# Optimization experiments

Measured on AMD Instinct MI355X. Metric: run time of the kernel, lower is better.

The kernel has to match this reference:

```python
import jax, jax.numpy as jnp
import numpy as np

MOMENTUM = 0.9
BN_EPS = 1e-5
NORM_EPS = 1e-12
NUM_CLASSES = 10000
DIM_MLP = 512
NUM_EXPERTS = 3
FEAT_DIM = 256
N = 4096


def _l2norm(x, axis=-1):
    # F.normalize: x / max(||x||, eps)
    n = jnp.sqrt(jnp.sum(x * x, axis=axis, keepdims=True))
    return x / jnp.maximum(n, NORM_EPS)


def setup_inputs() -> dict:
    key = jax.random.key(0)
    ks = jax.random.split(key, 8)
    feat_in = jax.random.normal(ks[0], (N, DIM_MLP * NUM_EXPERTS), dtype=jnp.float32)
    label = jax.random.randint(ks[1], (N,), 0, NUM_CLASSES, dtype=jnp.int32)
    # encoder params
    W1 = jax.random.normal(ks[2], (DIM_MLP * NUM_EXPERTS, DIM_MLP), dtype=jnp.float32) / np.sqrt(DIM_MLP * NUM_EXPERTS)
    b1 = jnp.zeros((DIM_MLP,), dtype=jnp.float32)
    gamma = jnp.ones((DIM_MLP,), dtype=jnp.float32)
    beta = jnp.zeros((DIM_MLP,), dtype=jnp.float32)
    W2 = jax.random.normal(ks[3], (DIM_MLP, FEAT_DIM), dtype=jnp.float32) / np.sqrt(DIM_MLP)
    b2 = jnp.zeros((FEAT_DIM,), dtype=jnp.float32)
    # memory bank buffer: randn then row-normalized (as in __init__)
    memory_pt = _l2norm(jax.random.normal(ks[4], (NUM_CLASSES, FEAT_DIM), dtype=jnp.float32))
    return {"feat_in": feat_in, "label": label, "W1": W1, "b1": b1,
            "gamma": gamma, "beta": beta, "W2": W2, "b2": b2,
            "memory_pt": memory_pt}


def _encoder(feat_in, W1, b1, gamma, beta, W2, b2):
    h = feat_in @ W1 + b1                       # [N, dim_mlp]
    # BatchNorm1d in training mode: batch statistics (biased variance)
    mu = jnp.mean(h, axis=0)
    var = jnp.mean((h - mu) ** 2, axis=0)
    h = (h - mu) * jax.lax.rsqrt(var + BN_EPS) * gamma + beta
    h = jax.nn.relu(h)
    out = h @ W2 + b2                           # [N, 256]
    return _l2norm(out, axis=1)


def _update_memory(memory_pt, feat, label):
    # Strictly sequential per-sample momentum update (order matters for
    # duplicate labels), each touched row renormalized — lax.scan recurrence.
    def step(mem, xy):
        x, y = xy
        pt = MOMENTUM * mem[y] + (1.0 - MOMENTUM) * x
        pt = _l2norm(pt, axis=0)
        return mem.at[y].set(pt), None
    mem, _ = jax.lax.scan(step, memory_pt, (feat, label))
    return mem


def reference(feat_in, label, W1, b1, gamma, beta, W2, b2, memory_pt):
    feat = _encoder(feat_in, W1, b1, gamma, beta, W2, b2)   # [N, 256], unit rows
    # memory_pt.detach(): no grad flows through the memory bank
    mem = _update_memory(jax.lax.stop_gradient(memory_pt),
                         jax.lax.stop_gradient(feat), label)
    mem = jax.lax.stop_gradient(mem)
    sim_logit = jnp.einsum('nc,kc->nk', feat, mem)          # [N, K]
    return sim_logit
```

## Files before the change

### kernel.cpp

```cpp
#include <hip/hip_runtime.h>
#include <stdint.h>

typedef _Float16 f16;
typedef _Float16 f16x2 __attribute__((ext_vector_type(2)));
typedef _Float16 f16x4 __attribute__((ext_vector_type(4)));
typedef _Float16 f16x8 __attribute__((ext_vector_type(8)));
typedef float f32x4 __attribute__((ext_vector_type(4)));

typedef __attribute__((address_space(1))) void gvoid;
typedef __attribute__((address_space(3))) void lvoid;

#define NROWS 4096
#define DIMIN 1536
#define DMLP 512
#define FDIM 256
#define NCLS 10000
#define NPAD 10112

__device__ __forceinline__ void load_lds16(const void* g, void* l) {
    __builtin_amdgcn_global_load_lds((gvoid*)g, (lvoid*)l, 16, 0, 0);
}

template<int TM, int TN>
__global__ __launch_bounds__(256) void gemm_t(
    const f16* __restrict__ A, const f16* __restrict__ Bt,
    float* __restrict__ C, const float* __restrict__ bias,
    int K, int ldc, int Nstore)
{
    constexpr int BK = 64;
    constexpr int AM = TM / 32;
    constexpr int AN = TN / 32;
    constexpr int CA = TM * 8;
    constexpr int CB = TN * 8;
    constexpr int RTOT = (CA + CB) / 256;

    __shared__ f16 As[TM * BK];
    __shared__ f16 Bs[TN * BK];

    const int tid  = threadIdx.x;
    const int lane = tid & 63;
    const int w    = tid >> 6;
    const int wm   = (w >> 1) * (TM / 2);
    const int wn   = (w & 1) * (TN / 2);
    const int row0 = blockIdx.x * TM;
    const int col0 = blockIdx.y * TN;
    const int quad = lane >> 4;
    const int r16  = lane & 15;

    f32x4 acc[AM][AN] = {};

    const f16* gsrc[RTOT];
    f16* ldst[RTOT];
#pragma unroll
    for (int r = 0; r < RTOT; ++r) {
        int c = tid + r * 256;
        bool isA = (c < CA);
        int cc = isA ? c : c - CA;
        int row = cc >> 3;
        int gs = (cc & 7) ^ (row & 7);
        gsrc[r] = (isA ? A + (size_t)(row0 + row) * K
                       : Bt + (size_t)(col0 + row) * K) + gs * 8;
        ldst[r] = (isA ? As : Bs) + cc * 8;
    }

    for (int k0 = 0; k0 < K; k0 += BK) {
#pragma unroll
        for (int r = 0; r < RTOT; ++r)
            load_lds16(gsrc[r] + k0, ldst[r]);
        __syncthreads();

#pragma unroll
        for (int ks = 0; ks < 2; ++ks) {
            f16x8 af[AM], bq[AN];
#pragma unroll
            for (int mi = 0; mi < AM; ++mi) {
                int row = wm + mi * 16 + r16;
                int slot = (ks * 4 + quad) ^ (r16 & 7);
                af[mi] = *(const f16x8*)&As[row * BK + slot * 8];
            }
#pragma unroll
            for (int ni = 0; ni < AN; ++ni) {
                int row = wn + ni * 16 + r16;
                int slot = (ks * 4 + quad) ^ (r16 & 7);
                bq[ni] = *(const f16x8*)&Bs[row * BK + slot * 8];
            }
#pragma unroll
            for (int mi = 0; mi < AM; ++mi)
#pragma unroll
                for (int ni = 0; ni < AN; ++ni)
                    acc[mi][ni] = __builtin_amdgcn_mfma_f32_16x16x32_f16(
                        af[mi], bq[ni], acc[mi][ni], 0, 0, 0);
        }
        __syncthreads();
    }

#pragma unroll
    for (int mi = 0; mi < AM; ++mi) {
#pragma unroll
        for (int ni = 0; ni < AN; ++ni) {
            int col = col0 + wn + ni * 16 + r16;
            if (col < Nstore) {
                float bv = bias ? bias[col] : 0.0f;
                int rowb = row0 + wm + mi * 16 + quad * 4;
#pragma unroll
                for (int r = 0; r < 4; ++r)
                    C[(size_t)(rowb + r) * ldc + col] = acc[mi][ni][r] + bv;
            }
        }
    }
}

__global__ void zero_k(float* __restrict__ p, int n) {
    int i = blockIdx.x * 256 + threadIdx.x;
    if (i < n) p[i] = 0.0f;
}

__global__ void f32_to_f16_k(const float* __restrict__ in, f16* __restrict__ out, int n4) {
    int i = blockIdx.x * 256 + threadIdx.x;
    if (i >= n4) return;
    float4 v = *(const float4*)&in[(size_t)i * 4];
    f16x4 o = {(f16)v.x, (f16)v.y, (f16)v.z, (f16)v.w};
    *(f16x4*)&out[(size_t)i * 4] = o;
}

__global__ void transpose_to_f16_k(const float* __restrict__ in, f16* __restrict__ out, int R, int C) {
    int idx = blockIdx.x * 256 + threadIdx.x;
    if (idx >= R * C) return;
    int n = idx / R, k = idx - n * R;
    out[idx] = (f16)in[(size_t)k * C + n];
}

__global__ void bn_stats_k(const float* __restrict__ h, float* __restrict__ sums, float* __restrict__ sqs) {
    int t = threadIdx.x, b = blockIdx.x;
    int c = t * 2;
    float s0 = 0.f, s1 = 0.f, q0 = 0.f, q1 = 0.f;
    for (int r = b; r < NROWS; r += 128) {
        float2 v = *(const float2*)&h[(size_t)r * DMLP + c];
        s0 += v.x; s1 += v.y; q0 += v.x * v.x; q1 += v.y * v.y;
    }
    atomicAdd(&sums[c], s0);
    atomicAdd(&sums[c + 1], s1);
    atomicAdd(&sqs[c], q0);
    atomicAdd(&sqs[c + 1], q1);
}

__global__ void bn_finish_k(const float* __restrict__ sums, const float* __restrict__ sqs,
                            const float* __restrict__ gamma, const float* __restrict__ beta,
                            float* __restrict__ scale, float* __restrict__ shift) {
    int c = blockIdx.x * 256 + threadIdx.x;
    if (c >= DMLP) return;
    const float inv_n = 1.0f / 4096.0f;
    float mu = sums[c] * inv_n;
    float var = fmaxf(sqs[c] * inv_n - mu * mu, 0.0f);
    float a = rsqrtf(var + 1e-5f) * gamma[c];
    scale[c] = a;
    shift[c] = beta[c] - mu * a;
}

__global__ void bn_apply_k(const float* __restrict__ h, const float* __restrict__ scale,
                           const float* __restrict__ shift, f16* __restrict__ out) {
    int i = blockIdx.x * 256 + threadIdx.x;
    int c = (i & 127) * 4;
    float4 v = *(const float4*)&h[(size_t)i * 4];
    float4 sc = *(const float4*)&scale[c];
    float4 sh = *(const float4*)&shift[c];
    f16x4 o = {(f16)fmaxf(v.x * sc.x + sh.x, 0.0f),
               (f16)fmaxf(v.y * sc.y + sh.y, 0.0f),
               (f16)fmaxf(v.z * sc.z + sh.z, 0.0f),
               (f16)fmaxf(v.w * sc.w + sh.w, 0.0f)};
    *(f16x4*)&out[(size_t)i * 4] = o;
}

__global__ void l2norm_k(const float* __restrict__ X, float* __restrict__ Y, f16* __restrict__ Yh) {
    int wv = (blockIdx.x * 256 + threadIdx.x) >> 6;
    int lane = threadIdx.x & 63;
    float4 v = *(const float4*)&X[(size_t)wv * FDIM + lane * 4];
    float s = v.x * v.x + v.y * v.y + v.z * v.z + v.w * v.w;
#pragma unroll
    for (int off = 32; off > 0; off >>= 1) s += __shfl_xor(s, off);
    float inv = 1.0f / fmaxf(sqrtf(s), 1e-12f);
    float4 o = {v.x * inv, v.y * inv, v.z * inv, v.w * inv};
    *(float4*)&Y[(size_t)wv * FDIM + lane * 4] = o;
    f16x4 oh = {(f16)o.x, (f16)o.y, (f16)o.z, (f16)o.w};
    *(f16x4*)&Yh[(size_t)wv * FDIM + lane * 4] = oh;
}

__global__ void chain_k(const int* __restrict__ label, const float* __restrict__ feat,
                        const float* __restrict__ mp, f16* __restrict__ memh) {
    int y = (blockIdx.x * 256 + threadIdx.x) >> 6;
    int lane = threadIdx.x & 63;
    float4 m = {0.f, 0.f, 0.f, 0.f};
    if (y < NCLS) {
        m = *(const float4*)&mp[(size_t)y * FDIM + lane * 4];
        for (int g = 0; g < 64; ++g) {
            int lab = label[g * 64 + lane];
            unsigned long long mask = __ballot(lab == y);
            while (mask) {
                int b = __builtin_ctzll(mask);
                mask &= mask - 1;
                int i = g * 64 + b;
                float4 x = *(const float4*)&feat[(size_t)i * FDIM + lane * 4];
                m.x = 0.9f * m.x + 0.1f * x.x;
                m.y = 0.9f * m.y + 0.1f * x.y;
                m.z = 0.9f * m.z + 0.1f * x.z;
                m.w = 0.9f * m.w + 0.1f * x.w;
                float s = m.x * m.x + m.y * m.y + m.z * m.z + m.w * m.w;
#pragma unroll
                for (int off = 32; off > 0; off >>= 1) s += __shfl_xor(s, off);
                float inv = 1.0f / fmaxf(sqrtf(s), 1e-12f);
                m.x *= inv; m.y *= inv; m.z *= inv; m.w *= inv;
            }
        }
    }
    f16x4 o = {(f16)m.x, (f16)m.y, (f16)m.z, (f16)m.w};
    *(f16x4*)&memh[(size_t)y * FDIM + lane * 4] = o;
}

extern "C" void kernel_launch(void* const* d_in, const int* in_sizes, int n_in,
                              void* d_out, int out_size, void* d_ws, size_t ws_size,
                              hipStream_t stream) {
    const float* feat_in = (const float*)d_in[0];
    const int*   label   = (const int*)d_in[1];
    const float* W1      = (const float*)d_in[2];
    const float* b1      = (const float*)d_in[3];
    const float* gamma   = (const float*)d_in[4];
    const float* beta    = (const float*)d_in[5];
    const float* W2      = (const float*)d_in[6];
    const float* b2      = (const float*)d_in[7];
    const float* mp      = (const float*)d_in[8];
    float* out = (float*)d_out;

    char* w = (char*)d_ws;
    f16* A1h   = (f16*)w;   w += (size_t)NROWS * DIMIN * 2;
    f16* W1t   = (f16*)w;   w += (size_t)DMLP * DIMIN * 2;
    f16* W2t   = (f16*)w;   w += (size_t)FDIM * DMLP * 2;
    float* h   = (float*)w; w += (size_t)NROWS * DMLP * 4;
    f16* h2    = (f16*)w;   w += (size_t)NROWS * DMLP * 2;
    float* out2= (float*)w; w += (size_t)NROWS * FDIM * 4;
    float* feat= (float*)w; w += (size_t)NROWS * FDIM * 4;
    f16* feath = (f16*)w;   w += (size_t)NROWS * FDIM * 2;
    f16* memh  = (f16*)w;   w += (size_t)NPAD * FDIM * 2;
    float* sums= (float*)w; w += DMLP * 4;
    float* sqs = (float*)w; w += DMLP * 4;
    float* bnsc= (float*)w; w += DMLP * 4;
    float* bnsh= (float*)w; w += DMLP * 4;

    zero_k<<<4, 256, 0, stream>>>(sums, 2 * DMLP);
    f32_to_f16_k<<<(NROWS * DIMIN / 4) / 256, 256, 0, stream>>>(feat_in, A1h, NROWS * DIMIN / 4);
    transpose_to_f16_k<<<(DIMIN * DMLP) / 256, 256, 0, stream>>>(W1, W1t, DIMIN, DMLP);
    transpose_to_f16_k<<<(DMLP * FDIM) / 256, 256, 0, stream>>>(W2, W2t, DMLP, FDIM);

    {
        dim3 g(NROWS / 64, DMLP / 64);
        gemm_t<64, 64><<<g, 256, 0, stream>>>(A1h, W1t, h, b1, DIMIN, DMLP, DMLP);
    }

    bn_stats_k<<<128, 256, 0, stream>>>(h, sums, sqs);
    bn_finish_k<<<2, 256, 0, stream>>>(sums, sqs, gamma, beta, bnsc, bnsh);
    bn_apply_k<<<(NROWS * DMLP / 4) / 256, 256, 0, stream>>>(h, bnsc, bnsh, h2);

    {
        dim3 g(NROWS / 64, FDIM / 64);
        gemm_t<64, 64><<<g, 256, 0, stream>>>(h2, W2t, out2, b2, DMLP, FDIM, FDIM);
    }

    l2norm_k<<<NROWS / 4, 256, 0, stream>>>(out2, feat, feath);

    chain_k<<<NPAD / 4, 256, 0, stream>>>(label, feat, mp, memh);

    {
        dim3 g(NROWS / 128, NPAD / 128);
        gemm_t<128, 128><<<g, 256, 0, stream>>>(feath, memh, out, nullptr, FDIM, NCLS, NCLS);
    }
}
```

Measured before the change: 331.6 us.

## Double-buffer GEMM LDS, fuse BN stats into GEMM epilogue, skip untouched memory rows

```diff
diff --git a/kernel.cpp b/kernel.cpp
--- a/kernel.cpp
+++ b/kernel.cpp
@@ -16,16 +16,18 @@
 #define FDIM 256
 #define NCLS 10000
 #define NPAD 10112
+#define NBMW 320
 
 __device__ __forceinline__ void load_lds16(const void* g, void* l) {
     __builtin_amdgcn_global_load_lds((gvoid*)g, (lvoid*)l, 16, 0, 0);
 }
 
-template<int TM, int TN>
+template<int TM, int TN, bool STATS, bool NT>
 __global__ __launch_bounds__(256) void gemm_t(
     const f16* __restrict__ A, const f16* __restrict__ Bt,
     float* __restrict__ C, const float* __restrict__ bias,
-    int K, int ldc, int Nstore)
+    int K, int ldc, int Nstore,
+    float* __restrict__ sums, float* __restrict__ sqs)
 {
     constexpr int BK = 64;
     constexpr int AM = TM / 32;
@@ -33,9 +35,10 @@
     constexpr int CA = TM * 8;
     constexpr int CB = TN * 8;
     constexpr int RTOT = (CA + CB) / 256;
-
-    __shared__ f16 As[TM * BK];
-    __shared__ f16 Bs[TN * BK];
+    constexpr int SPAN = (TM + TN) * BK;
+    static_assert(CA % 256 == 0, "A/B staging split must be round-aligned");
+
+    __shared__ f16 smem[2 * SPAN];
 
     const int tid  = threadIdx.x;
     const int lane = tid & 63;
@@ -50,7 +53,7 @@
     f32x4 acc[AM][AN] = {};
 
     const f16* gsrc[RTOT];
-    f16* ldst[RTOT];
+    int ldsoff[RTOT];
 #pragma unroll
     for (int r = 0; r < RTOT; ++r) {
         int c = tid + r * 256;
@@ -60,15 +63,27 @@
         int gs = (cc & 7) ^ (row & 7);
         gsrc[r] = (isA ? A + (size_t)(row0 + row) * K
                        : Bt + (size_t)(col0 + row) * K) + gs * 8;
-        ldst[r] = (isA ? As : Bs) + cc * 8;
-    }
-
-    for (int k0 = 0; k0 < K; k0 += BK) {
-#pragma unroll
-        for (int r = 0; r < RTOT; ++r)
-            load_lds16(gsrc[r] + k0, ldst[r]);
-        __syncthreads();
-
+        ldsoff[r] = (isA ? 0 : TM * BK) + cc * 8;
+    }
+
+    const int nt = K / BK;
+
+#pragma unroll
+    for (int r = 0; r < RTOT; ++r)
+        load_lds16(gsrc[r], smem + ldsoff[r]);
+    __syncthreads();
+
+    int buf = 0;
+    for (int t = 0; t < nt; ++t) {
+        if (t + 1 < nt) {
+            const int k0 = (t + 1) * BK;
+            const int o = (buf ^ 1) * SPAN;
+#pragma unroll
+            for (int r = 0; r < RTOT; ++r)
+                load_lds16(gsrc[r] + k0, smem + o + ldsoff[r]);
+        }
+        const f16* As = smem + buf * SPAN;
+        const f16* Bs = As + TM * BK;
 #pragma unroll
         for (int ks = 0; ks < 2; ++ks) {
             f16x8 af[AM], bq[AN];
@@ -92,19 +107,35 @@
                         af[mi], bq[ni], acc[mi][ni], 0, 0, 0);
         }
         __syncthreads();
-    }
-
-#pragma unroll
-    for (int mi = 0; mi < AM; ++mi) {
-#pragma unroll
-        for (int ni = 0; ni < AN; ++ni) {
-            int col = col0 + wn + ni * 16 + r16;
-            if (col < Nstore) {
-                float bv = bias ? bias[col] : 0.0f;
+        buf ^= 1;
+    }
+
+#pragma unroll
+    for (int ni = 0; ni < AN; ++ni) {
+        int col = col0 + wn + ni * 16 + r16;
+        float bv = bias ? bias[col] : 0.0f;
+        float s = 0.0f, q = 0.0f;
+        if (col < Nstore) {
+#pragma unroll
+            for (int mi = 0; mi < AM; ++mi) {
                 int rowb = row0 + wm + mi * 16 + quad * 4;
 #pragma unroll
-                for (int r = 0; r < 4; ++r)
-                    C[(size_t)(rowb + r) * ldc + col] = acc[mi][ni][r] + bv;
+                for (int r = 0; r < 4; ++r) {
+                    float v = acc[mi][ni][r] + bv;
+                    if constexpr (NT)
+                        __builtin_nontemporal_store(v, &C[(size_t)(rowb + r) * ldc + col]);
+                    else
+                        C[(size_t)(rowb + r) * ldc + col] = v;
+                    if constexpr (STATS) { s += v; q += v * v; }
+                }
+            }
+        }
+        if constexpr (STATS) {
+            s += __shfl_xor(s, 16); s += __shfl_xor(s, 32);
+            q += __shfl_xor(q, 16); q += __shfl_xor(q, 32);
+            if (quad == 0) {
+                atomicAdd(&sums[col], s);
+                atomicAdd(&sqs[col], q);
             }
         }
     }
@@ -123,25 +154,24 @@
     *(f16x4*)&out[(size_t)i * 4] = o;
 }
 
-__global__ void transpose_to_f16_k(const float* __restrict__ in, f16* __restrict__ out, int R, int C) {
-    int idx = blockIdx.x * 256 + threadIdx.x;
-    if (idx >= R * C) return;
-    int n = idx / R, k = idx - n * R;
-    out[idx] = (f16)in[(size_t)k * C + n];
-}
-
-__global__ void bn_stats_k(const float* __restrict__ h, float* __restrict__ sums, float* __restrict__ sqs) {
-    int t = threadIdx.x, b = blockIdx.x;
-    int c = t * 2;
-    float s0 = 0.f, s1 = 0.f, q0 = 0.f, q1 = 0.f;
-    for (int r = b; r < NROWS; r += 128) {
-        float2 v = *(const float2*)&h[(size_t)r * DMLP + c];
-        s0 += v.x; s1 += v.y; q0 += v.x * v.x; q1 += v.y * v.y;
-    }
-    atomicAdd(&sums[c], s0);
-    atomicAdd(&sums[c + 1], s1);
-    atomicAdd(&sqs[c], q0);
-    atomicAdd(&sqs[c + 1], q1);
+__global__ void transpose_f16_tile_k(const float* __restrict__ in, f16* __restrict__ out,
+                                     int R, int C) {
+    __shared__ float t[32][33];
+    int tx = threadIdx.x & 31, ty = threadIdx.x >> 5;
+    int c0 = blockIdx.x * 32, r0 = blockIdx.y * 32;
+#pragma unroll
+    for (int k = 0; k < 4; ++k)
+        t[ty + k * 8][tx] = in[(size_t)(r0 + ty + k * 8) * C + c0 + tx];
+    __syncthreads();
+#pragma unroll
+    for (int k = 0; k < 4; ++k)
+        out[(size_t)(c0 + ty + k * 8) * R + r0 + tx] = (f16)t[tx][ty + k * 8];
+}
+
+__global__ void touch_k(const int* __restrict__ label, unsigned int* __restrict__ bm) {
+    int i = blockIdx.x * 256 + threadIdx.x;
+    int y = label[i];
+    atomicOr(&bm[y >> 5], 1u << (y & 31));
 }
 
 __global__ void bn_finish_k(const float* __restrict__ sums, const float* __restrict__ sqs,
@@ -186,29 +216,32 @@
 }
 
 __global__ void chain_k(const int* __restrict__ label, const float* __restrict__ feat,
-                        const float* __restrict__ mp, f16* __restrict__ memh) {
+                        const float* __restrict__ mp, const unsigned int* __restrict__ bm,
+                        f16* __restrict__ memh) {
     int y = (blockIdx.x * 256 + threadIdx.x) >> 6;
     int lane = threadIdx.x & 63;
     float4 m = {0.f, 0.f, 0.f, 0.f};
     if (y < NCLS) {
         m = *(const float4*)&mp[(size_t)y * FDIM + lane * 4];
-        for (int g = 0; g < 64; ++g) {
-            int lab = label[g * 64 + lane];
-            unsigned long long mask = __ballot(lab == y);
-            while (mask) {
-                int b = __builtin_ctzll(mask);
-                mask &= mask - 1;
-                int i = g * 64 + b;
-                float4 x = *(const float4*)&feat[(size_t)i * FDIM + lane * 4];
-                m.x = 0.9f * m.x + 0.1f * x.x;
-                m.y = 0.9f * m.y + 0.1f * x.y;
-                m.z = 0.9f * m.z + 0.1f * x.z;
-                m.w = 0.9f * m.w + 0.1f * x.w;
-                float s = m.x * m.x + m.y * m.y + m.z * m.z + m.w * m.w;
-#pragma unroll
-                for (int off = 32; off > 0; off >>= 1) s += __shfl_xor(s, off);
-                float inv = 1.0f / fmaxf(sqrtf(s), 1e-12f);
-                m.x *= inv; m.y *= inv; m.z *= inv; m.w *= inv;
+        if ((bm[y >> 5] >> (y & 31)) & 1u) {
+            for (int g = 0; g < 64; ++g) {
+                int lab = label[g * 64 + lane];
+                unsigned long long mask = __ballot(lab == y);
+                while (mask) {
+                    int b = __builtin_ctzll(mask);
+                    mask &= mask - 1;
+                    int i = g * 64 + b;
+                    float4 x = *(const float4*)&feat[(size_t)i * FDIM + lane * 4];
+                    m.x = 0.9f * m.x + 0.1f * x.x;
+                    m.y = 0.9f * m.y + 0.1f * x.y;
+                    m.z = 0.9f * m.z + 0.1f * x.z;
+                    m.w = 0.9f * m.w + 0.1f * x.w;
+                    float s = m.x * m.x + m.y * m.y + m.z * m.z + m.w * m.w;
+#pragma unroll
+                    for (int off = 32; off > 0; off >>= 1) s += __shfl_xor(s, off);
+                    float inv = 1.0f / fmaxf(sqrtf(s), 1e-12f);
+                    m.x *= inv; m.y *= inv; m.z *= inv; m.w *= inv;
+                }
             }
         }
     }
@@ -242,34 +275,42 @@
     f16* memh  = (f16*)w;   w += (size_t)NPAD * FDIM * 2;
     float* sums= (float*)w; w += DMLP * 4;
     float* sqs = (float*)w; w += DMLP * 4;
+    unsigned int* bm = (unsigned int*)w; w += NBMW * 4;
     float* bnsc= (float*)w; w += DMLP * 4;
     float* bnsh= (float*)w; w += DMLP * 4;
 
-    zero_k<<<4, 256, 0, stream>>>(sums, 2 * DMLP);
+    zero_k<<<6, 256, 0, stream>>>(sums, 2 * DMLP + NBMW);
+    touch_k<<<NROWS / 256, 256, 0, stream>>>(label, bm);
     f32_to_f16_k<<<(NROWS * DIMIN / 4) / 256, 256, 0, stream>>>(feat_in, A1h, NROWS * DIMIN / 4);
-    transpose_to_f16_k<<<(DIMIN * DMLP) / 256, 256, 0, stream>>>(W1, W1t, DIMIN, DMLP);
-    transpose_to_f16_k<<<(DMLP * FDIM) / 256, 256, 0, stream>>>(W2, W2t, DMLP, FDIM);
-
     {
-        dim3 g(NROWS / 64, DMLP / 64);
-        gemm_t<64, 64><<<g, 256, 0, stream>>>(A1h, W1t, h, b1, DIMIN, DMLP, DMLP);
-    }
-
-    bn_stats_k<<<128, 256, 0, stream>>>(h, sums, sqs);
+        dim3 g1(DMLP / 32, DIMIN / 32);
+        transpose_f16_tile_k<<<g1, 256, 0, stream>>>(W1, W1t, DIMIN, DMLP);
+        dim3 g2(FDIM / 32, DMLP / 32);
+        transpose_f16_tile_k<<<g2, 256, 0, stream>>>(W2, W2t, DMLP, FDIM);
+    }
+
+    {
+        dim3 g(NROWS / 128, DMLP / 64);
+        gemm_t<128, 64, true, false><<<g, 256, 0, stream>>>(
+            A1h, W1t, h, b1, DIMIN, DMLP, DMLP, sums, sqs);
+    }
+
     bn_finish_k<<<2, 256, 0, stream>>>(sums, sqs, gamma, beta, bnsc, bnsh);
     bn_apply_k<<<(NROWS * DMLP / 4) / 256, 256, 0, stream>>>(h, bnsc, bnsh, h2);
 
     {
         dim3 g(NROWS / 64, FDIM / 64);
-        gemm_t<64, 64><<<g, 256, 0, stream>>>(h2, W2t, out2, b2, DMLP, FDIM, FDIM);
+        gemm_t<64, 64, false, false><<<g, 256, 0, stream>>>(
+            h2, W2t, out2, b2, DMLP, FDIM, FDIM, nullptr, nullptr);
     }
 
     l2norm_k<<<NROWS / 4, 256, 0, stream>>>(out2, feat, feath);
 
-    chain_k<<<NPAD / 4, 256, 0, stream>>>(label, feat, mp, memh);
+    chain_k<<<NPAD / 4, 256, 0, stream>>>(label, feat, mp, bm, memh);
 
     {
         dim3 g(NROWS / 128, NPAD / 128);
-        gemm_t<128, 128><<<g, 256, 0, stream>>>(feath, memh, out, nullptr, FDIM, NCLS, NCLS);
-    }
-}
+        gemm_t<128, 128, false, true><<<g, 256, 0, stream>>>(
+            feath, memh, out, nullptr, FDIM, NCLS, NCLS, nullptr, nullptr);
+    }
+}
```

After: 295.1 us. -11.0%, faster.
